# Optimization experiments

Hardware: AMD Instinct MI355X
Metric: run time of the kernel (lower is better)

Reference implementation:

```python
import jax, jax.numpy as jnp
import numpy as np

N = 50000   # nodes
D = 3       # relations
E = 800000  # edges per relation
F_IN, F_HID = 300, 128
LEAKY = 0.2

def setup_inputs() -> dict:
    key = jax.random.key(0)
    ks = jax.random.split(key, 8)
    feat = jax.random.normal(ks[0], (N, F_IN), jnp.float32)
    rows = jax.random.randint(ks[1], (D, E), 0, N, jnp.int32)
    cols = jax.random.randint(ks[2], (D, E), 0, N, jnp.int32)
    # xavier_uniform-style scales
    s1 = (6.0 / (F_IN + F_HID)) ** 0.5
    s2 = (6.0 / (F_HID + F_HID)) ** 0.5
    w1 = jax.random.uniform(ks[3], (F_IN, F_HID), jnp.float32, -s1, s1)
    w2 = jax.random.uniform(ks[4], (F_HID, F_HID), jnp.float32, -s2, s2)
    b1 = jnp.zeros((F_HID,), jnp.float32)
    b2 = jnp.zeros((F_HID,), jnp.float32)
    a_att = jnp.ones((D,), jnp.float32)
    r_att = jnp.ones((D,), jnp.float32)
    label_idx = jax.random.randint(ks[5], (1000,), 0, N, jnp.int32)
    return dict(feat=feat, w1=w1, b1=b1, w2=w2, b2=b2, a_att=a_att,
                r_att=r_att, rows=rows, cols=cols, label_idx=label_idx)

def _spmm_rownorm(r, c, x):
    # y = A_norm @ x, A in COO (r,c) with value 1, rows normalized by row degree
    deg = jax.ops.segment_sum(jnp.ones_like(r, jnp.float32), r, num_segments=N)
    inv = jnp.where(deg > 0, 1.0 / jnp.maximum(deg, 1.0), 0.0)
    msgs = inv[r][:, None] * x[c]          # [E, F] gathered, weighted messages
    return jax.ops.segment_sum(msgs, r, num_segments=N)

def _graph_conv(x, w, b, rows, cols, att):
    support = x @ w + b                     # [N, F_out]
    a = jax.nn.softmax(att)                 # softmax over relations
    out = jnp.zeros((N, w.shape[1]), support.dtype)
    for i in range(D):                      # small fixed relation count
        out = out + _spmm_rownorm(rows[i], cols[i], support) * a[i]
    out = jnp.where(out > 0, out, LEAKY * out)   # LeakyReLU(0.2)
    nrm = jnp.maximum(jnp.linalg.norm(out, axis=1, keepdims=True), 1e-12)
    return out / nrm                        # F.normalize (L2, per row)

def reference(feat, w1, b1, w2, b2, a_att, r_att, rows, cols, label_idx):
    # layer 0: a_adj (forward edges), layer 1: r_adj (transposed edges)
    x = _graph_conv(feat, w1, b1, rows, cols, a_att)
    x = _graph_conv(x, w2, b2, cols, rows, r_att)
    return x[label_idx, :]
```

## Files before the change

### kernel.cpp

```cpp
#include <hip/hip_runtime.h>
#include <hip/hip_bf16.h>
#include <hip/hip_fp16.h>

#define LEAKY_SLOPE 0.2f
#define HIST_C 85
#define HIST_THREADS 1024
#define CG 5
#define CGC 17
#define KP 320

typedef __attribute__((ext_vector_type(8))) short bf16x8;
typedef __attribute__((ext_vector_type(4))) float f32x4;
typedef _Float16 h2 __attribute__((ext_vector_type(2)));

__device__ __forceinline__ unsigned short f2bf(float f) {
  __hip_bfloat16 h = __float2bfloat16(f);
  return *(unsigned short*)&h;
}
__device__ __forceinline__ float bf2f(unsigned short u) {
  return __uint_as_float(((unsigned)u) << 16);
}
__device__ __forceinline__ unsigned short f2h(float f) {
  __half h = __float2half(f);
  return *(unsigned short*)&h;
}


__global__ __launch_bounds__(256) void k_setup(int* __restrict__ z, int zn2,
                                               const float* __restrict__ w1,
                                               unsigned short* __restrict__ WThi,
                                               unsigned short* __restrict__ WTlo, int K,
                                               const float* __restrict__ a_att,
                                               const float* __restrict__ r_att,
                                               float* __restrict__ a_soft) {
  int i = blockIdx.x * 256 + threadIdx.x;
  if (i < zn2) z[i] = 0;
  if (i < 128 * KP) {
    int n = i / KP, k = i - n * KP;
    float f = (k < K) ? w1[(size_t)k * 128 + n] : 0.f;
    unsigned short hi = f2bf(f);
    WThi[i] = hi;
    WTlo[i] = f2bf(f - bf2f(hi));
  }
  if (i == 0) {
    float m = fmaxf(fmaxf(a_att[0], a_att[1]), a_att[2]);
    float e0 = expf(a_att[0] - m), e1 = expf(a_att[1] - m), e2 = expf(a_att[2] - m);
    float s = 1.0f / (e0 + e1 + e2);
    a_soft[0] = e0 * s; a_soft[1] = e1 * s; a_soft[2] = e2 * s;
    m = fmaxf(fmaxf(r_att[0], r_att[1]), r_att[2]);
    e0 = expf(r_att[0] - m); e1 = expf(r_att[1] - m); e2 = expf(r_att[2] - m);
    s = 1.0f / (e0 + e1 + e2);
    a_soft[3] = e0 * s; a_soft[4] = e1 * s; a_soft[5] = e2 * s;
  }
}

__global__ __launch_bounds__(256) void k_lab(const int* __restrict__ lidx,
                                             unsigned* __restrict__ bm,
                                             int* __restrict__ lab_of, int L) {
  int i = blockIdx.x * 256 + threadIdx.x;
  if (i < L) {
    int n = lidx[i];
    atomicOr(&bm[n >> 5], 1u << (n & 31));
    atomicMax(&lab_of[n], i + 1);
  }
}

__global__ __launch_bounds__(HIST_THREADS) void k_hist(const int* __restrict__ rows,
                                                       const int* __restrict__ cols,
                                                       const unsigned* __restrict__ bm,
                                                       int* __restrict__ deg2,
                                                       unsigned* __restrict__ flag_bm,
                                                       int* __restrict__ hcnt,
                                                       int* __restrict__ hsrc, int* __restrict__ hpack,
                                                       unsigned char* __restrict__ rank8,
                                                       unsigned* __restrict__ histc,
                                                       int N, int E, int chunk) {
  extern __shared__ unsigned sh[];
  __shared__ int s_cnt;
  int WN4 = (N + 3) >> 2;
  unsigned* hist = sh;
  int tid = threadIdx.x;
  int cidx = blockIdx.x, rel = blockIdx.y;

  for (int i = tid; i < WN4; i += HIST_THREADS) hist[i] = 0;
  if (tid == 0) s_cnt = 0;
  __syncthreads();

  int estart = cidx * chunk;
  int eend = min(estart + chunk, E);
  int rbase = (rel * HIST_C + cidx) * chunk;
  const int* rp = rows + (size_t)rel * E;
  const int* cp = cols + (size_t)rel * E;
  for (int base = estart + tid * 8; base < eend; base += 8 * HIST_THREADS) {
    int r[8], c[8];
    bool full = (base + 7) < eend;
    if (full) {
      *(int4*)&r[0] = *(const int4*)&rp[base];
      *(int4*)&r[4] = *(const int4*)&rp[base + 4];
      *(int4*)&c[0] = *(const int4*)&cp[base];
      *(int4*)&c[4] = *(const int4*)&cp[base + 4];
    } else {
#pragma unroll
      for (int j = 0; j < 8; ++j) {
        int e = base + j;
        r[j] = (e < eend) ? rp[e] : 0;
        c[j] = (e < eend) ? cp[e] : 0;
      }
    }
    unsigned rk0 = 0, rk1 = 0;
#pragma unroll
    for (int j = 0; j < 8; ++j) {
      if (base + j < eend) {
        int rj = r[j], cj = c[j];
        unsigned old = atomicAdd(&hist[rj >> 2], 1u << (8 * (rj & 3)));
        unsigned rv = (old >> (8 * (rj & 3))) & 0xFFu;
        if (j < 4) rk0 |= rv << (8 * j); else rk1 |= rv << (8 * (j - 4));
        if ((bm[cj >> 5] >> (cj & 31)) & 1u) {
          atomicAdd(&deg2[rel * N + cj], 1);
          atomicOr(&flag_bm[rj >> 5], 1u << (rj & 31));
          int p = atomicAdd(&s_cnt, 1);
          hsrc[rbase + p] = rj;
          hpack[rbase + p] = (rel << 20) | cj;
        }
      }
    }
    if (full) {
      *(uint2*)&rank8[(size_t)rel * E + base] = make_uint2(rk0, rk1);
    } else {
#pragma unroll
      for (int j = 0; j < 8; ++j) {
        if (base + j < eend) {
          unsigned rv = (j < 4) ? (rk0 >> (8 * j)) : (rk1 >> (8 * (j - 4)));
          rank8[(size_t)rel * E + base + j] = (unsigned char)(rv & 0xFFu);
        }
      }
    }
  }
  __syncthreads();
  if (tid == 0) hcnt[rel * HIST_C + cidx] = s_cnt;
  unsigned* dst = &histc[(size_t)(rel * HIST_C + cidx) * WN4];
  for (int i = tid; i < WN4; i += HIST_THREADS) dst[i] = hist[i];
}

__global__ __launch_bounds__(256) void k_red_a(const unsigned* __restrict__ histc,
                                               ushort4* __restrict__ psum, int WN4) {
  int word = blockIdx.x * 256 + threadIdx.x;
  if (word >= WN4) return;
  int rc = blockIdx.y;
  int rel = rc / CG, cg = rc - rel * CG;
  size_t hb = ((size_t)rel * HIST_C + cg * CGC) * WN4 + word;
  int s0 = 0, s1 = 0, s2 = 0, s3 = 0;
#pragma unroll
  for (int i = 0; i < CGC; ++i) {
    unsigned w = histc[hb + (size_t)i * WN4];
    s0 += w & 0xFFu; s1 += (w >> 8) & 0xFFu; s2 += (w >> 16) & 0xFFu; s3 += w >> 24;
  }
  psum[(size_t)rc * WN4 + word] =
      make_ushort4((unsigned short)s0, (unsigned short)s1,
                   (unsigned short)s2, (unsigned short)s3);
}

__global__ __launch_bounds__(256) void k_red_b(const ushort4* __restrict__ psum,
                                               ushort4* __restrict__ cgb,
                                               const float* __restrict__ a_soft,
                                               float* __restrict__ inv1,
                                               int* __restrict__ row_ptr,
                                               int* __restrict__ chunk_sums,
                                               int N, int WN4) {
  __shared__ int sd[256];
  int tid = threadIdx.x;
  int t = blockIdx.x * 256 + tid;
  int run[4] = {0, 0, 0, 0};
  bool act = t < WN4;
  int d0 = 4 * t;
  if (act) {
#pragma unroll
    for (int rel = 0; rel < 3; ++rel) {
      int start[4];
#pragma unroll
      for (int j = 0; j < 4; ++j) start[j] = run[j];
#pragma unroll
      for (int cg = 0; cg < CG; ++cg) {
        size_t idx = (size_t)(rel * CG + cg) * WN4 + t;
        ushort4 p = psum[idx];
        cgb[idx] = make_ushort4((unsigned short)run[0], (unsigned short)run[1],
                                (unsigned short)run[2], (unsigned short)run[3]);
        run[0] += p.x; run[1] += p.y; run[2] += p.z; run[3] += p.w;
      }
      float a = a_soft[rel];
#pragma unroll
      for (int j = 0; j < 4; ++j) {
        int d = d0 + j;
        if (d < N) inv1[rel * N + d] = a / (float)max(run[j] - start[j], 1);
      }
    }
  }
  int v[4];
#pragma unroll
  for (int j = 0; j < 4; ++j) v[j] = (act && d0 + j < N) ? run[j] : 0;
  sd[tid] = v[0] + v[1] + v[2] + v[3];
  __syncthreads();
  for (int off = 1; off < 256; off <<= 1) {
    int x = (tid >= off) ? sd[tid - off] : 0;
    __syncthreads();
    sd[tid] += x;
    __syncthreads();
  }
  int runp = tid ? sd[tid - 1] : 0;
#pragma unroll
  for (int j = 0; j < 4; ++j) {
    int n = d0 + j;
    if (n < N) row_ptr[n] = runp;
    runp += v[j];
  }
  if (tid == 255) chunk_sums[blockIdx.x] = sd[255];
}

__global__ __launch_bounds__(256) void k_red_c(const unsigned* __restrict__ histc,
                                               const ushort4* __restrict__ cgb,
                                               unsigned* __restrict__ cbase_w, int WN4) {
  int word = blockIdx.x * 256 + threadIdx.x;
  if (word >= WN4) return;
  int rc = blockIdx.y;
  int rel = rc / CG, cg = rc - rel * CG;
  ushort4 b = cgb[(size_t)rc * WN4 + word];
  unsigned r0 = b.x, r1 = b.y, r2 = b.z, r3 = b.w;
  size_t hb = ((size_t)rel * HIST_C + cg * CGC) * WN4 + word;
#pragma unroll
  for (int i = 0; i < CGC; ++i) {
    unsigned w = histc[hb + (size_t)i * WN4];
    cbase_w[hb + (size_t)i * WN4] =
        (r0 & 0xFFu) | ((r1 & 0xFFu) << 8) | ((r2 & 0xFFu) << 16) | ((r3 & 0xFFu) << 24);
    r0 += w & 0xFFu; r1 += (w >> 8) & 0xFFu; r2 += (w >> 16) & 0xFFu; r3 += w >> 24;
  }
}

__global__ __launch_bounds__(256) void k_scan23(int* __restrict__ row_ptr,
                                                const int* __restrict__ chunk_sums,
                                                int nchunks,
                                                const unsigned* __restrict__ flag_bm,
                                                int* __restrict__ wl, int* __restrict__ wl_cnt,
                                                int N) {
  __shared__ int s_cnt, s_base;
  int tid = threadIdx.x;
  int lane = tid & 63;
  int mine = (lane < nchunks) ? chunk_sums[lane] : 0;
  int vsc = mine;
  for (int off = 1; off < 64; off <<= 1) {
    int x = __shfl_up(vsc, off, 64);
    if (lane >= off) vsc += x;
  }
  int c = (blockIdx.x * 256) >> 10;
  int coff = (c == 0) ? 0 : __shfl(vsc, c - 1, 64);
  int total = __shfl(vsc, nchunks - 1, 64);
  if (blockIdx.x == 0 && tid == 0) row_ptr[N] = total;
  if (tid == 0) s_cnt = 0;
  __syncthreads();
  int n = blockIdx.x * 256 + tid;
  bool f = false;
  int p = 0;
  if (n < N) {
    row_ptr[n] += coff;
    f = (flag_bm[n >> 5] >> (n & 31)) & 1u;
    if (f) p = atomicAdd(&s_cnt, 1);
  }
  __syncthreads();
  if (tid == 0 && s_cnt > 0) s_base = atomicAdd(wl_cnt, s_cnt);
  __syncthreads();
  if (f) wl[s_base + p] = n;
}


__global__ __launch_bounds__(256) void k_scatter(const int* __restrict__ rows,
                                                 const int* __restrict__ cols,
                                                 const int* __restrict__ row_ptr,
                                                 const unsigned char* __restrict__ cbase,
                                                 const unsigned char* __restrict__ rank8,
                                                 const unsigned* __restrict__ flag_bm,
                                                 unsigned* __restrict__ esrc,
                                                 int N, int E, int chunk) {
  int e0 = (blockIdx.x * 256 + threadIdx.x) * 4;
  int rel = blockIdx.y;
  if (e0 >= E) return;
  const int* rp = rows + (size_t)rel * E;
  const int* cp = cols + (size_t)rel * E;
  int r[4], c[4];
  unsigned rk;
  if (e0 + 3 < E) {
    *(int4*)r = *(const int4*)&rp[e0];
    *(int4*)c = *(const int4*)&cp[e0];
    rk = *(const unsigned*)&rank8[(size_t)rel * E + e0];
  } else {
    rk = 0;
#pragma unroll
    for (int j = 0; j < 4; ++j) {
      int e = e0 + j;
      r[j] = (e < E) ? rp[e] : 0;
      c[j] = (e < E) ? cp[e] : 0;
      if (e < E) rk |= (unsigned)rank8[(size_t)rel * E + e] << (8 * j);
    }
  }
  int NP4 = ((N + 3) >> 2) * 4;
  int c0 = e0 / chunk;
  int rem = e0 - c0 * chunk;
#pragma unroll
  for (int j = 0; j < 4; ++j) {
    if (e0 + j >= E) break;
    int d = r[j];
    if (!((flag_bm[d >> 5] >> (d & 31)) & 1u)) continue;
    int cch = (rem + j >= chunk) ? c0 + 1 : c0;
    int pos = row_ptr[d] + (int)cbase[(size_t)(rel * HIST_C + cch) * NP4 + d]
            + (int)((rk >> (8 * j)) & 0xFFu);
    esrc[pos] = ((unsigned)rel << 16) | (unsigned)c[j];
  }
}


__global__ __launch_bounds__(256) void k_gemm1(const float* __restrict__ A,
                                               const unsigned short* __restrict__ WThi,
                                               const unsigned short* __restrict__ WTlo,
                                               const float* __restrict__ bias,
                                               unsigned short* __restrict__ outh,
                                               int M, int K) {
  __shared__ unsigned short sAhi[64 * 64];
  __shared__ unsigned short sWhi[128 * 64], sWlo[128 * 64];
  char* pAhi = (char*)sAhi;
  char* pWhi = (char*)sWhi; char* pWlo = (char*)sWlo;
  int tid = threadIdx.x;
  int wave = tid >> 6, lane = tid & 63;
  int row0 = blockIdx.x * 64;
  f32x4 acc[8];
#pragma unroll
  for (int i = 0; i < 8; ++i) acc[i] = (f32x4){0.f, 0.f, 0.f, 0.f};

  for (int c = 0; c < 5; ++c) {
    int k0 = c * 64;
    __syncthreads();
    for (int i = tid; i < 1024; i += 256) {
      int r = i >> 4, q = i & 15;
      int gr = row0 + r, gk = k0 + q * 4;
      float4 v = make_float4(0.f, 0.f, 0.f, 0.f);
      if (gr < M && gk < K) v = *(const float4*)&A[(size_t)gr * K + gk];
      unsigned h0 = (unsigned)f2bf(v.x) | ((unsigned)f2bf(v.y) << 16);
      unsigned h1 = (unsigned)f2bf(v.z) | ((unsigned)f2bf(v.w) << 16);
      int byte = (r * 128 + q * 8) ^ ((r & 7) << 4);
      *(uint2*)(pAhi + byte) = make_uint2(h0, h1);
    }
    for (int i = tid; i < 1024; i += 256) {
      int n = i >> 3, u = i & 7;
      size_t g = (size_t)n * KP + k0 + u * 8;
      int byte = (n * 128 + u * 16) ^ ((n & 7) << 4);
      *(uint4*)(pWhi + byte) = *(const uint4*)&WThi[g];
      *(uint4*)(pWlo + byte) = *(const uint4*)&WTlo[g];
    }
    __syncthreads();
#pragma unroll
    for (int ks = 0; ks < 2; ++ks) {
      int m = wave * 16 + (lane & 15);
      int kb = ks * 32 + (lane >> 4) * 8;
      bf16x8 ahi = *(const bf16x8*)(pAhi + ((m * 128 + kb * 2) ^ ((m & 7) << 4)));
#pragma unroll
      for (int nt = 0; nt < 8; ++nt) {
        int n = nt * 16 + (lane & 15);
        int wb = (n * 128 + kb * 2) ^ ((n & 7) << 4);
        bf16x8 bhi = *(const bf16x8*)(pWhi + wb);
        bf16x8 blo = *(const bf16x8*)(pWlo + wb);
        acc[nt] = __builtin_amdgcn_mfma_f32_16x16x32_bf16(ahi, bhi, acc[nt], 0, 0, 0);
        acc[nt] = __builtin_amdgcn_mfma_f32_16x16x32_bf16(ahi, blo, acc[nt], 0, 0, 0);
      }
    }
  }
#pragma unroll
  for (int nt = 0; nt < 8; ++nt) {
    int n = nt * 16 + (lane & 15);
    float bv = bias[n];
#pragma unroll
    for (int j = 0; j < 4; ++j) {
      int m = row0 + wave * 16 + (lane >> 4) * 4 + j;
      if (m < M) outh[(size_t)m * 128 + n] = f2h(acc[nt][j] + bv);
    }
  }
}


__global__ __launch_bounds__(256) void k_agg_norm(const unsigned short* __restrict__ supp,
                                                  const int* __restrict__ row_ptr,
                                                  const unsigned* __restrict__ esrc,
                                                  const float* __restrict__ inv1,
                                                  const int* __restrict__ wl,
                                                  const int* __restrict__ wl_cnt,
                                                  unsigned short* __restrict__ out, int N) {
  int wi = blockIdx.x * 4 + (threadIdx.x >> 6);
  if (wi >= wl_cnt[0]) return;
  int row = __builtin_amdgcn_readfirstlane(wl[wi]);
  int lane = threadIdx.x & 63;
  int grp = lane >> 4;
  int l16 = lane & 15;
  int s = row_ptr[row], e = row_ptr[row + 1];
  _Float16 w0h = (_Float16)inv1[row];
  _Float16 w1h = (_Float16)inv1[N + row];
  _Float16 w2h = (_Float16)inv1[2 * N + row];
  float acc[8] = {};
  for (int j = s; j < e; j += 8) {
    int j0 = j + grp, j1 = j + 4 + grp;
    bool a0 = j0 < e, a1 = j1 < e;
    unsigned u0 = esrc[a0 ? j0 : s];
    unsigned u1 = esrc[a1 ? j1 : s];
    int rel0 = (int)(u0 >> 16), src0 = (int)(u0 & 0xFFFFu);
    int rel1 = (int)(u1 >> 16), src1 = (int)(u1 & 0xFFFFu);
    _Float16 wa = (rel0 == 0) ? w0h : ((rel0 == 1) ? w1h : w2h);
    _Float16 wb = (rel1 == 0) ? w0h : ((rel1 == 1) ? w1h : w2h);
    if (!a0) wa = (_Float16)0.f;
    if (!a1) wb = (_Float16)0.f;
    h2 wpk;
    wpk[0] = wa; wpk[1] = wb;
    uint4 p0 = *(const uint4*)&supp[(size_t)src0 * 128 + l16 * 8];
    uint4 p1 = *(const uint4*)&supp[(size_t)src1 * 128 + l16 * 8];
#pragma unroll
    for (int q = 0; q < 4; ++q) {
      unsigned a = (&p0.x)[q];
      unsigned b = (&p1.x)[q];
      unsigned lo = __builtin_amdgcn_perm(b, a, 0x05040100u);
      unsigned hi = __builtin_amdgcn_perm(b, a, 0x07060302u);
      acc[2 * q]     = __builtin_amdgcn_fdot2(__builtin_bit_cast(h2, lo), wpk,
                                              acc[2 * q], false);
      acc[2 * q + 1] = __builtin_amdgcn_fdot2(__builtin_bit_cast(h2, hi), wpk,
                                              acc[2 * q + 1], false);
    }
  }
#pragma unroll
  for (int i = 0; i < 8; ++i) {
    acc[i] += __shfl_xor(acc[i], 16, 64);
    acc[i] += __shfl_xor(acc[i], 32, 64);
  }
  float ss = 0.f;
#pragma unroll
  for (int i = 0; i < 8; ++i) {
    acc[i] = acc[i] > 0.f ? acc[i] : LEAKY_SLOPE * acc[i];
    ss += acc[i] * acc[i];
  }
#pragma unroll
  for (int m = 1; m < 16; m <<= 1) ss += __shfl_xor(ss, m, 64);
  float inv = 1.0f / fmaxf(sqrtf(ss), 1e-12f);
  if (lane < 16) {
    unsigned pk[4];
#pragma unroll
    for (int q = 0; q < 4; ++q) {
      pk[q] = (unsigned)f2bf(acc[2 * q] * inv) |
              ((unsigned)f2bf(acc[2 * q + 1] * inv) << 16);
    }
    *(uint4*)&out[(size_t)row * 128 + l16 * 8] = make_uint4(pk[0], pk[1], pk[2], pk[3]);
  }
}

__global__ __launch_bounds__(1024) void k_cnt2(const int* __restrict__ lidx,
                                               const int* __restrict__ lab_of,
                                               const int* __restrict__ deg2,
                                               const float* __restrict__ a_soft,
                                               int* __restrict__ hb_ptr,
                                               int* __restrict__ cnt2,
                                               int* __restrict__ fill2,
                                               float* __restrict__ sumw, int N, int L) {
  __shared__ int sd[1024];
  int t = threadIdx.x;
  int cnt = 0;
  if (t < L) {
    int d = lidx[t];
    int c0 = deg2[d], c1 = deg2[N + d], c2 = deg2[2 * N + d];
    if (lab_of[d] == t + 1) cnt = c0 + c1 + c2;
    sumw[t] = a_soft[3] * (c0 > 0 ? 1.f : 0.f) +
              a_soft[4] * (c1 > 0 ? 1.f : 0.f) +
              a_soft[5] * (c2 > 0 ? 1.f : 0.f);
  }
  sd[t] = cnt;
  __syncthreads();
  for (int off = 1; off < 1024; off <<= 1) {
    int v = (t >= off) ? sd[t - off] : 0;
    __syncthreads();
    sd[t] += v;
    __syncthreads();
  }
  if (t < L) {
    int base = sd[t] - cnt;
    hb_ptr[t] = base;
    fill2[t] = base;
    cnt2[t] = cnt;
  }
}

__global__ __launch_bounds__(256) void k_scatter2(const int* __restrict__ hsrc,
                                                  const int* __restrict__ hpack,
                                                  const int* __restrict__ hcnt,
                                                  const int* __restrict__ lab_of,
                                                  int* __restrict__ fill2,
                                                  unsigned* __restrict__ hdata, int chunk) {
  int reg = blockIdx.x;
  int cnt = hcnt[reg];
  int rbase = reg * chunk;
  for (int i = threadIdx.x; i < cnt; i += 256) {
    int src = hsrc[rbase + i], pk = hpack[rbase + i];
    int rel = pk >> 20, d = pk & 0xFFFFF;
    int li = lab_of[d] - 1;
    int pos = atomicAdd(&fill2[li], 1);
    hdata[pos] = ((unsigned)rel << 16) | (unsigned)src;
  }
}

__global__ __launch_bounds__(256) void k_agg2(const unsigned short* __restrict__ h1,
                                              const int* __restrict__ hb_ptr,
                                              const int* __restrict__ cnt2,
                                              const unsigned* __restrict__ hdata,
                                              const int* __restrict__ lidx,
                                              const int* __restrict__ deg2,
                                              const float* __restrict__ a_soft,
                                              float* __restrict__ aggh, int N, int L) {
  int wv = blockIdx.x * 4 + (threadIdx.x >> 6);
  if (wv >= L) return;
  int li = __builtin_amdgcn_readfirstlane(wv);
  int lane = threadIdx.x & 63;
  int grp = lane >> 4, l16 = lane & 15;
  int d = lidx[li];
  int s = hb_ptr[li], e = s + cnt2[li];
  float w0 = a_soft[3] / (float)max(deg2[d], 1);
  float w1 = a_soft[4] / (float)max(deg2[N + d], 1);
  float w2 = a_soft[5] / (float)max(deg2[2 * N + d], 1);
  float acc[8] = {};
  for (int j = s; j < e; j += 4) {
    int jj = j + grp;
    bool act = jj < e;
    unsigned u = hdata[act ? jj : s];
    int rel = (int)(u >> 16);
    int src = (int)(u & 0xFFFFu);
    float w = (rel == 0) ? w0 : ((rel == 1) ? w1 : w2);
    if (!act) w = 0.f;
    uint4 pv = *(const uint4*)&h1[(size_t)src * 128 + l16 * 8];
#pragma unroll
    for (int q = 0; q < 4; ++q) {
      unsigned p = (&pv.x)[q];
      acc[2 * q]     += w * __uint_as_float(p << 16);
      acc[2 * q + 1] += w * __uint_as_float(p & 0xFFFF0000u);
    }
  }
#pragma unroll
  for (int i = 0; i < 8; ++i) {
    acc[i] += __shfl_xor(acc[i], 16, 64);
    acc[i] += __shfl_xor(acc[i], 32, 64);
  }
  if (lane < 16) {
    *(float4*)&aggh[(size_t)li * 128 + l16 * 8] =
        make_float4(acc[0], acc[1], acc[2], acc[3]);
    *(float4*)&aggh[(size_t)li * 128 + l16 * 8 + 4] =
        make_float4(acc[4], acc[5], acc[6], acc[7]);
  }
}

__global__ __launch_bounds__(256) void k_final(const float* __restrict__ aggh,
                                               const float* __restrict__ W2,
                                               const float* __restrict__ b2,
                                               const float* __restrict__ sumw,
                                               const int* __restrict__ lidx,
                                               const int* __restrict__ lab_of,
                                               float* __restrict__ out, int L) {
  __shared__ float sW[64][128];
  __shared__ float sA[32][64];
  __shared__ int s_c[32];
  __shared__ float s_sw[32];
  int tid = threadIdx.x;
  int wave = tid >> 6, lane = tid & 63;
  int lane2 = lane * 2;
  int row0 = blockIdx.x * 32;
  if (tid < 32) {
    int gr = row0 + tid;
    int c = 0; float sw = 0.f;
    if (gr < L) {
      c = lab_of[lidx[gr]] - 1;
      if (c < 0) c = 0;
      sw = sumw[gr];
    }
    s_c[tid] = c; s_sw[tid] = sw;
  }
  __syncthreads();
  float acc[8][2] = {};
  for (int k0 = 0; k0 < 128; k0 += 64) {
    __syncthreads();
    for (int i = tid; i < 64 * 32; i += 256) {
      int kk = i >> 5, c4 = i & 31;
      ((float4*)&sW[kk][0])[c4] = ((const float4*)&W2[(size_t)(k0 + kk) * 128])[c4];
    }
    for (int i = tid; i < 32 * 16; i += 256) {
      int r = i >> 4, kq = i & 15;
      int gr = row0 + r;
      float4 v = make_float4(0.f, 0.f, 0.f, 0.f);
      if (gr < L) v = ((const float4*)&aggh[(size_t)s_c[r] * 128 + k0])[kq];
      ((float4*)&sA[r][0])[kq] = v;
    }
    __syncthreads();
    const float* ap = &sA[wave * 8][0];
    for (int kk = 0; kk < 64; kk += 2) {
      float2 w0 = *(const float2*)&sW[kk][lane2];
      float2 w1 = *(const float2*)&sW[kk + 1][lane2];
#pragma unroll
      for (int r = 0; r < 8; ++r) {
        float2 av = *(const float2*)&ap[r * 64 + kk];
        acc[r][0] += av.x * w0.x + av.y * w1.x;
        acc[r][1] += av.x * w0.y + av.y * w1.y;
      }
    }
  }
  float2 bv = *(const float2*)&b2[lane2];
#pragma unroll
  for (int r = 0; r < 8; ++r) {
    int gr = row0 + wave * 8 + r;
    float sw = s_sw[wave * 8 + r];
    float ax = acc[r][0] + bv.x * sw;
    float ay = acc[r][1] + bv.y * sw;
    ax = ax > 0.f ? ax : LEAKY_SLOPE * ax;
    ay = ay > 0.f ? ay : LEAKY_SLOPE * ay;
    float ss = ax * ax + ay * ay;
#pragma unroll
    for (int m = 1; m < 64; m <<= 1) ss += __shfl_xor(ss, m, 64);
    float inv = 1.0f / fmaxf(sqrtf(ss), 1e-12f);
    if (gr < L) {
      *(float2*)&out[(size_t)gr * 128 + lane2] = make_float2(ax * inv, ay * inv);
    }
  }
}


extern "C" void kernel_launch(void* const* d_in, const int* in_sizes, int n_in,
                              void* d_out, int out_size, void* d_ws, size_t ws_size,
                              hipStream_t stream) {
  const float* feat  = (const float*)d_in[0];
  const float* w1    = (const float*)d_in[1];
  const float* b1    = (const float*)d_in[2];
  const float* w2    = (const float*)d_in[3];
  const float* b2    = (const float*)d_in[4];
  const float* a_att = (const float*)d_in[5];
  const float* r_att = (const float*)d_in[6];
  const int* rows    = (const int*)d_in[7];
  const int* cols    = (const int*)d_in[8];
  const int* lidx    = (const int*)d_in[9];

  const int F = 128;
  int K1 = in_sizes[1] / F;
  int N  = in_sizes[0] / K1;
  int E  = in_sizes[7] / 3;
  int L  = in_sizes[9];
  float* outp = (float*)d_out;
  (void)n_in; (void)out_size; (void)ws_size;

  int WN4 = (N + 3) >> 2;
  int chunk = (((E + HIST_C - 1) / HIST_C) + 7) & ~7;

  char* base = (char*)d_ws;
  size_t off = 0;
  auto take = [&](size_t bytes) -> void* {
    size_t cur = (off + 255) & ~(size_t)255;
    off = cur + bytes;
    return (void*)(base + cur);
  };
  unsigned short* supph = (unsigned short*)take((size_t)N * F * 2);
  unsigned short* h1 = (unsigned short*)take((size_t)N * F * 2);
  unsigned* esrc = (unsigned*)take((size_t)3 * E * 4);
  unsigned char* rank8 = (unsigned char*)take((size_t)3 * E);
  unsigned* histc = (unsigned*)take((size_t)3 * HIST_C * WN4 * 4);
  unsigned* cbase_w = (unsigned*)take((size_t)3 * HIST_C * WN4 * 4);
  ushort4* psum = (ushort4*)take((size_t)15 * WN4 * 8);
  ushort4* cgb  = (ushort4*)take((size_t)15 * WN4 * 8);
  float* inv1  = (float*)take((size_t)3 * N * 4);
  int* row_ptr = (int*)take((size_t)(N + 1) * 4);
  int* wl      = (int*)take((size_t)N * 4);
  int* hsrc  = (int*)take((size_t)3 * HIST_C * chunk * 4);
  int* hpack = (int*)take((size_t)3 * HIST_C * chunk * 4);
  unsigned short* WThi = (unsigned short*)take((size_t)128 * KP * 2);
  unsigned short* WTlo = (unsigned short*)take((size_t)128 * KP * 2);
  float* aggh = (float*)take((size_t)1024 * F * 4);
  int nb = (N + 31) / 32;
  int zn2 = 3 * N + 2 * nb + 1 + N;
  int* deg2 = (int*)take((size_t)zn2 * 4);
  unsigned* bm = (unsigned*)(deg2 + 3 * N);
  unsigned* flag_bm = bm + nb;
  int* wl_cnt = (int*)(flag_bm + nb);
  int* lab_of = wl_cnt + 1;
  int* hcnt = (int*)take((size_t)(3 * HIST_C + 1) * 4);
  int* hb_ptr = (int*)take(1024 * 4);
  int* cnt2   = (int*)take(1024 * 4);
  int* fill2  = (int*)take(1024 * 4);
  float* sumw = (float*)take(1024 * 4);
  float* a_soft = (float*)take(64);
  int* chunk_sums = (int*)take(256);
  unsigned* hdata = esrc;

  int nchunks = (N + 1023) / 1024;
  int nwb = (WN4 + 255) / 256;
  size_t shbytes = (size_t)WN4 * 4;
  hipFuncSetAttribute((const void*)k_hist, hipFuncAttributeMaxDynamicSharedMemorySize,
                      (int)shbytes);

  int setup_n = max(zn2, 128 * KP);
  hipLaunchKernelGGL(k_setup, dim3((setup_n + 255) / 256), dim3(256), 0, stream,
                     deg2, zn2, w1, WThi, WTlo, K1, a_att, r_att, a_soft);
  hipLaunchKernelGGL(k_lab, dim3((L + 255) / 256), dim3(256), 0, stream,
                     lidx, bm, lab_of, L);
  hipLaunchKernelGGL(k_hist, dim3(HIST_C, 3), dim3(HIST_THREADS), shbytes, stream,
                     rows, cols, bm, deg2, flag_bm, hcnt, hsrc, hpack, rank8, histc,
                     N, E, chunk);
  hipLaunchKernelGGL(k_gemm1, dim3((N + 63) / 64), dim3(256), 0, stream,
                     feat, WThi, WTlo, b1, supph, N, K1);
  hipLaunchKernelGGL(k_red_a, dim3(nwb, 15), dim3(256), 0, stream, histc, psum, WN4);
  hipLaunchKernelGGL(k_red_b, dim3(nwb), dim3(256), 0, stream,
                     psum, cgb, a_soft, inv1, row_ptr, chunk_sums, N, WN4);
  hipLaunchKernelGGL(k_red_c, dim3(nwb, 15), dim3(256), 0, stream, histc, cgb, cbase_w, WN4);
  hipLaunchKernelGGL(k_scan23, dim3((N + 255) / 256), dim3(256), 0, stream,
                     row_ptr, chunk_sums, nchunks, flag_bm, wl, wl_cnt, N);
  hipLaunchKernelGGL(k_scatter, dim3((E + 1023) / 1024, 3), dim3(256), 0, stream,
                     rows, cols, row_ptr, (const unsigned char*)cbase_w, rank8, flag_bm,
                     esrc, N, E, chunk);
  hipLaunchKernelGGL(k_agg_norm, dim3((N + 3) / 4), dim3(256), 0, stream,
                     supph, row_ptr, esrc, inv1, wl, wl_cnt, h1, N);
  hipLaunchKernelGGL(k_cnt2, dim3(1), dim3(1024), 0, stream,
                     lidx, lab_of, deg2, a_soft, hb_ptr, cnt2, fill2, sumw, N, L);
  hipLaunchKernelGGL(k_scatter2, dim3(3 * HIST_C), dim3(256), 0, stream,
                     hsrc, hpack, hcnt, lab_of, fill2, hdata, chunk);
  hipLaunchKernelGGL(k_agg2, dim3((L + 3) / 4), dim3(256), 0, stream,
                     h1, hb_ptr, cnt2, hdata, lidx, deg2, a_soft, aggh, N, L);
  hipLaunchKernelGGL(k_final, dim3((L + 31) / 32), dim3(256), 0, stream,
                     aggh, w2, b2, sumw, lidx, lab_of, outp, L);
}
```

Before: 236.3 us.

## Fuse first-layer GEMM into histogram kernel with persistent dynamic tile scheduling

The histogram kernel and the first feature GEMM become one kernel. Each of the 255 histogram blocks, after finishing its chunk, pulls 256-row GEMM tiles from a global atomic counter and reuses the same shared memory. This removes a separate launch and lets the GEMM run on blocks as they free up, hiding histogram tail imbalance. The trade-off is that only 255 large blocks of 1024 threads do the GEMM, so occupancy is lower than the old 782 small blocks, and the per-tile atomic adds serialisation.

```diff
diff --git a/kernel.cpp b/kernel.cpp
--- a/kernel.cpp
+++ b/kernel.cpp
@@ -65,81 +65,150 @@
   }
 }
 
-__global__ __launch_bounds__(HIST_THREADS) void k_hist(const int* __restrict__ rows,
-                                                       const int* __restrict__ cols,
-                                                       const unsigned* __restrict__ bm,
-                                                       int* __restrict__ deg2,
-                                                       unsigned* __restrict__ flag_bm,
-                                                       int* __restrict__ hcnt,
-                                                       int* __restrict__ hsrc, int* __restrict__ hpack,
-                                                       unsigned char* __restrict__ rank8,
-                                                       unsigned* __restrict__ histc,
-                                                       int N, int E, int chunk) {
+__global__ __launch_bounds__(HIST_THREADS) void k_hist_gemm(
+    const int* __restrict__ rows, const int* __restrict__ cols,
+    const unsigned* __restrict__ bm, int* __restrict__ deg2,
+    unsigned* __restrict__ flag_bm, int* __restrict__ hcnt,
+    int* __restrict__ hsrc, int* __restrict__ hpack,
+    unsigned char* __restrict__ rank8, unsigned* __restrict__ histc,
+    int N, int E, int chunk,
+    const float* __restrict__ A, const unsigned short* __restrict__ WThi,
+    const unsigned short* __restrict__ WTlo, const float* __restrict__ bias,
+    unsigned short* __restrict__ outh, int M, int K, int* __restrict__ gctr) {
   extern __shared__ unsigned sh[];
   __shared__ int s_cnt;
+  __shared__ int s_tile;
   int WN4 = (N + 3) >> 2;
-  unsigned* hist = sh;
   int tid = threadIdx.x;
-  int cidx = blockIdx.x, rel = blockIdx.y;
-
-  for (int i = tid; i < WN4; i += HIST_THREADS) hist[i] = 0;
-  if (tid == 0) s_cnt = 0;
-  __syncthreads();
-
-  int estart = cidx * chunk;
-  int eend = min(estart + chunk, E);
-  int rbase = (rel * HIST_C + cidx) * chunk;
-  const int* rp = rows + (size_t)rel * E;
-  const int* cp = cols + (size_t)rel * E;
-  for (int base = estart + tid * 8; base < eend; base += 8 * HIST_THREADS) {
-    int r[8], c[8];
-    bool full = (base + 7) < eend;
-    if (full) {
-      *(int4*)&r[0] = *(const int4*)&rp[base];
-      *(int4*)&r[4] = *(const int4*)&rp[base + 4];
-      *(int4*)&c[0] = *(const int4*)&cp[base];
-      *(int4*)&c[4] = *(const int4*)&cp[base + 4];
-    } else {
-#pragma unroll
-      for (int j = 0; j < 8; ++j) {
-        int e = base + j;
-        r[j] = (e < eend) ? rp[e] : 0;
-        c[j] = (e < eend) ? cp[e] : 0;
-      }
-    }
-    unsigned rk0 = 0, rk1 = 0;
-#pragma unroll
-    for (int j = 0; j < 8; ++j) {
-      if (base + j < eend) {
-        int rj = r[j], cj = c[j];
-        unsigned old = atomicAdd(&hist[rj >> 2], 1u << (8 * (rj & 3)));
-        unsigned rv = (old >> (8 * (rj & 3))) & 0xFFu;
-        if (j < 4) rk0 |= rv << (8 * j); else rk1 |= rv << (8 * (j - 4));
-        if ((bm[cj >> 5] >> (cj & 31)) & 1u) {
-          atomicAdd(&deg2[rel * N + cj], 1);
-          atomicOr(&flag_bm[rj >> 5], 1u << (rj & 31));
-          int p = atomicAdd(&s_cnt, 1);
-          hsrc[rbase + p] = rj;
-          hpack[rbase + p] = (rel << 20) | cj;
+
+  {
+    unsigned* hist = sh;
+    int cidx = blockIdx.x % HIST_C, rel = blockIdx.x / HIST_C;
+
+    for (int i = tid; i < WN4; i += HIST_THREADS) hist[i] = 0;
+    if (tid == 0) s_cnt = 0;
+    __syncthreads();
+
+    int estart = cidx * chunk;
+    int eend = min(estart + chunk, E);
+    int rbase = (rel * HIST_C + cidx) * chunk;
+    const int* rp = rows + (size_t)rel * E;
+    const int* cp = cols + (size_t)rel * E;
+    for (int base = estart + tid * 8; base < eend; base += 8 * HIST_THREADS) {
+      int r[8], c[8];
+      bool full = (base + 7) < eend;
+      if (full) {
+        *(int4*)&r[0] = *(const int4*)&rp[base];
+        *(int4*)&r[4] = *(const int4*)&rp[base + 4];
+        *(int4*)&c[0] = *(const int4*)&cp[base];
+        *(int4*)&c[4] = *(const int4*)&cp[base + 4];
+      } else {
+#pragma unroll
+        for (int j = 0; j < 8; ++j) {
+          int e = base + j;
+          r[j] = (e < eend) ? rp[e] : 0;
+          c[j] = (e < eend) ? cp[e] : 0;
         }
       }
-    }
-    if (full) {
-      *(uint2*)&rank8[(size_t)rel * E + base] = make_uint2(rk0, rk1);
-    } else {
+      unsigned rk0 = 0, rk1 = 0;
 #pragma unroll
       for (int j = 0; j < 8; ++j) {
         if (base + j < eend) {
-          unsigned rv = (j < 4) ? (rk0 >> (8 * j)) : (rk1 >> (8 * (j - 4)));
-          rank8[(size_t)rel * E + base + j] = (unsigned char)(rv & 0xFFu);
+          int rj = r[j], cj = c[j];
+          unsigned old = atomicAdd(&hist[rj >> 2], 1u << (8 * (rj & 3)));
+          unsigned rv = (old >> (8 * (rj & 3))) & 0xFFu;
+          if (j < 4) rk0 |= rv << (8 * j); else rk1 |= rv << (8 * (j - 4));
+          if ((bm[cj >> 5] >> (cj & 31)) & 1u) {
+            atomicAdd(&deg2[rel * N + cj], 1);
+            atomicOr(&flag_bm[rj >> 5], 1u << (rj & 31));
+            int p = atomicAdd(&s_cnt, 1);
+            hsrc[rbase + p] = rj;
+            hpack[rbase + p] = (rel << 20) | cj;
+          }
         }
       }
-    }
-  }
-  __syncthreads();
-  if (tid == 0) hcnt[rel * HIST_C + cidx] = s_cnt;
-  unsigned* dst = &histc[(size_t)(rel * HIST_C + cidx) * WN4];
-  for (int i = tid; i < WN4; i += HIST_THREADS) dst[i] = hist[i];
+      if (full) {
+        *(uint2*)&rank8[(size_t)rel * E + base] = make_uint2(rk0, rk1);
+      } else {
+#pragma unroll
+        for (int j = 0; j < 8; ++j) {
+          if (base + j < eend) {
+            unsigned rv = (j < 4) ? (rk0 >> (8 * j)) : (rk1 >> (8 * (j - 4)));
+            rank8[(size_t)rel * E + base + j] = (unsigned char)(rv & 0xFFu);
+          }
+        }
+      }
+    }
+    __syncthreads();
+    if (tid == 0) hcnt[rel * HIST_C + cidx] = s_cnt;
+    unsigned* dst = &histc[(size_t)(rel * HIST_C + cidx) * WN4];
+    for (int i = tid; i < WN4; i += HIST_THREADS) dst[i] = hist[i];
+  }
+
+  char* pAhi = (char*)sh;
+  char* pWhi = (char*)sh + 32768;
+  char* pWlo = (char*)sh + 49152;
+  int wave = tid >> 6, lane = tid & 63;
+  int tiles = (M + 255) >> 8;
+  while (true) {
+    __syncthreads();
+    if (tid == 0) s_tile = atomicAdd(gctr, 1);
+    __syncthreads();
+    int tile = s_tile;
+    if (tile >= tiles) break;
+    int row0 = tile << 8;
+    f32x4 acc[8];
+#pragma unroll
+    for (int i = 0; i < 8; ++i) acc[i] = (f32x4){0.f, 0.f, 0.f, 0.f};
+
+    for (int cc = 0; cc < 5; ++cc) {
+      int k0 = cc * 64;
+      __syncthreads();
+      for (int i = tid; i < 4096; i += HIST_THREADS) {
+        int r = i >> 4, q = i & 15;
+        int gr = row0 + r, gk = k0 + q * 4;
+        float4 v = make_float4(0.f, 0.f, 0.f, 0.f);
+        if (gr < M && gk < K) v = *(const float4*)&A[(size_t)gr * K + gk];
+        unsigned h0 = (unsigned)f2bf(v.x) | ((unsigned)f2bf(v.y) << 16);
+        unsigned h1 = (unsigned)f2bf(v.z) | ((unsigned)f2bf(v.w) << 16);
+        int byte = (r * 128 + q * 8) ^ ((r & 7) << 4);
+        *(uint2*)(pAhi + byte) = make_uint2(h0, h1);
+      }
+      {
+        int n = tid >> 3, u = tid & 7;
+        size_t g = (size_t)n * KP + k0 + u * 8;
+        int byte = (n * 128 + u * 16) ^ ((n & 7) << 4);
+        *(uint4*)(pWhi + byte) = *(const uint4*)&WThi[g];
+        *(uint4*)(pWlo + byte) = *(const uint4*)&WTlo[g];
+      }
+      __syncthreads();
+#pragma unroll
+      for (int ks = 0; ks < 2; ++ks) {
+        int m = wave * 16 + (lane & 15);
+        int kb = ks * 32 + (lane >> 4) * 8;
+        bf16x8 ahi = *(const bf16x8*)(pAhi + ((m * 128 + kb * 2) ^ ((m & 7) << 4)));
+#pragma unroll
+        for (int nt = 0; nt < 8; ++nt) {
+          int n = nt * 16 + (lane & 15);
+          int wb = (n * 128 + kb * 2) ^ ((n & 7) << 4);
+          bf16x8 bhi = *(const bf16x8*)(pWhi + wb);
+          bf16x8 blo = *(const bf16x8*)(pWlo + wb);
+          acc[nt] = __builtin_amdgcn_mfma_f32_16x16x32_bf16(ahi, bhi, acc[nt], 0, 0, 0);
+          acc[nt] = __builtin_amdgcn_mfma_f32_16x16x32_bf16(ahi, blo, acc[nt], 0, 0, 0);
+        }
+      }
+    }
+#pragma unroll
+    for (int nt = 0; nt < 8; ++nt) {
+      int n = nt * 16 + (lane & 15);
+      float bv = bias[n];
+#pragma unroll
+      for (int j = 0; j < 4; ++j) {
+        int m = row0 + wave * 16 + (lane >> 4) * 4 + j;
+        if (m < M) outh[(size_t)m * 128 + n] = f2h(acc[nt][j] + bv);
+      }
+    }
+  }
 }
 
 __global__ __launch_bounds__(256) void k_red_a(const unsigned* __restrict__ histc,
@@ -312,73 +381,6 @@
     int pos = row_ptr[d] + (int)cbase[(size_t)(rel * HIST_C + cch) * NP4 + d]
             + (int)((rk >> (8 * j)) & 0xFFu);
     esrc[pos] = ((unsigned)rel << 16) | (unsigned)c[j];
-  }
-}
-
-
-__global__ __launch_bounds__(256) void k_gemm1(const float* __restrict__ A,
-                                               const unsigned short* __restrict__ WThi,
-                                               const unsigned short* __restrict__ WTlo,
-                                               const float* __restrict__ bias,
-                                               unsigned short* __restrict__ outh,
-                                               int M, int K) {
-  __shared__ unsigned short sAhi[64 * 64];
-  __shared__ unsigned short sWhi[128 * 64], sWlo[128 * 64];
-  char* pAhi = (char*)sAhi;
-  char* pWhi = (char*)sWhi; char* pWlo = (char*)sWlo;
-  int tid = threadIdx.x;
-  int wave = tid >> 6, lane = tid & 63;
-  int row0 = blockIdx.x * 64;
-  f32x4 acc[8];
-#pragma unroll
-  for (int i = 0; i < 8; ++i) acc[i] = (f32x4){0.f, 0.f, 0.f, 0.f};
-
-  for (int c = 0; c < 5; ++c) {
-    int k0 = c * 64;
-    __syncthreads();
-    for (int i = tid; i < 1024; i += 256) {
-      int r = i >> 4, q = i & 15;
-      int gr = row0 + r, gk = k0 + q * 4;
-      float4 v = make_float4(0.f, 0.f, 0.f, 0.f);
-      if (gr < M && gk < K) v = *(const float4*)&A[(size_t)gr * K + gk];
-      unsigned h0 = (unsigned)f2bf(v.x) | ((unsigned)f2bf(v.y) << 16);
-      unsigned h1 = (unsigned)f2bf(v.z) | ((unsigned)f2bf(v.w) << 16);
-      int byte = (r * 128 + q * 8) ^ ((r & 7) << 4);
-      *(uint2*)(pAhi + byte) = make_uint2(h0, h1);
-    }
-    for (int i = tid; i < 1024; i += 256) {
-      int n = i >> 3, u = i & 7;
-      size_t g = (size_t)n * KP + k0 + u * 8;
-      int byte = (n * 128 + u * 16) ^ ((n & 7) << 4);
-      *(uint4*)(pWhi + byte) = *(const uint4*)&WThi[g];
-      *(uint4*)(pWlo + byte) = *(const uint4*)&WTlo[g];
-    }
-    __syncthreads();
-#pragma unroll
-    for (int ks = 0; ks < 2; ++ks) {
-      int m = wave * 16 + (lane & 15);
-      int kb = ks * 32 + (lane >> 4) * 8;
-      bf16x8 ahi = *(const bf16x8*)(pAhi + ((m * 128 + kb * 2) ^ ((m & 7) << 4)));
-#pragma unroll
-      for (int nt = 0; nt < 8; ++nt) {
-        int n = nt * 16 + (lane & 15);
-        int wb = (n * 128 + kb * 2) ^ ((n & 7) << 4);
-        bf16x8 bhi = *(const bf16x8*)(pWhi + wb);
-        bf16x8 blo = *(const bf16x8*)(pWlo + wb);
-        acc[nt] = __builtin_amdgcn_mfma_f32_16x16x32_bf16(ahi, bhi, acc[nt], 0, 0, 0);
-        acc[nt] = __builtin_amdgcn_mfma_f32_16x16x32_bf16(ahi, blo, acc[nt], 0, 0, 0);
-      }
-    }
-  }
-#pragma unroll
-  for (int nt = 0; nt < 8; ++nt) {
-    int n = nt * 16 + (lane & 15);
-    float bv = bias[n];
-#pragma unroll
-    for (int j = 0; j < 4; ++j) {
-      int m = row0 + wave * 16 + (lane >> 4) * 4 + j;
-      if (m < M) outh[(size_t)m * 128 + n] = f2h(acc[nt][j] + bv);
-    }
   }
 }
 
@@ -676,12 +678,13 @@
   unsigned short* WTlo = (unsigned short*)take((size_t)128 * KP * 2);
   float* aggh = (float*)take((size_t)1024 * F * 4);
   int nb = (N + 31) / 32;
-  int zn2 = 3 * N + 2 * nb + 1 + N;
+  int zn2 = 3 * N + 2 * nb + 2 + N;
   int* deg2 = (int*)take((size_t)zn2 * 4);
   unsigned* bm = (unsigned*)(deg2 + 3 * N);
   unsigned* flag_bm = bm + nb;
   int* wl_cnt = (int*)(flag_bm + nb);
-  int* lab_of = wl_cnt + 1;
+  int* gctr = wl_cnt + 1;
+  int* lab_of = gctr + 1;
   int* hcnt = (int*)take((size_t)(3 * HIST_C + 1) * 4);
   int* hb_ptr = (int*)take(1024 * 4);
   int* cnt2   = (int*)take(1024 * 4);
@@ -693,20 +696,18 @@
 
   int nchunks = (N + 1023) / 1024;
   int nwb = (WN4 + 255) / 256;
-  size_t shbytes = (size_t)WN4 * 4;
-  hipFuncSetAttribute((const void*)k_hist, hipFuncAttributeMaxDynamicSharedMemorySize,
-                      (int)shbytes);
+  size_t shbytes = 65536;
+  hipFuncSetAttribute((const void*)k_hist_gemm,
+                      hipFuncAttributeMaxDynamicSharedMemorySize, (int)shbytes);
 
   int setup_n = max(zn2, 128 * KP);
   hipLaunchKernelGGL(k_setup, dim3((setup_n + 255) / 256), dim3(256), 0, stream,
                      deg2, zn2, w1, WThi, WTlo, K1, a_att, r_att, a_soft);
   hipLaunchKernelGGL(k_lab, dim3((L + 255) / 256), dim3(256), 0, stream,
                      lidx, bm, lab_of, L);
-  hipLaunchKernelGGL(k_hist, dim3(HIST_C, 3), dim3(HIST_THREADS), shbytes, stream,
+  hipLaunchKernelGGL(k_hist_gemm, dim3(3 * HIST_C), dim3(HIST_THREADS), shbytes, stream,
                      rows, cols, bm, deg2, flag_bm, hcnt, hsrc, hpack, rank8, histc,
-                     N, E, chunk);
-  hipLaunchKernelGGL(k_gemm1, dim3((N + 63) / 64), dim3(256), 0, stream,
-                     feat, WThi, WTlo, b1, supph, N, K1);
+                     N, E, chunk, feat, WThi, WTlo, b1, supph, N, K1, gctr);
   hipLaunchKernelGGL(k_red_a, dim3(nwb, 15), dim3(256), 0, stream, histc, psum, WN4);
   hipLaunchKernelGGL(k_red_b, dim3(nwb), dim3(256), 0, stream,
                      psum, cgb, a_soft, inv1, row_ptr, chunk_sums, N, WN4);
```

After: 296.3 us. +25.4%, slower.
